# Performance work log

Hardware: AMD Instinct MI355X
Metric: run time of the kernel (lower is better)

## Reference

```python
import jax, jax.numpy as jnp
import numpy as np

NEG = -1000000000.0
EPS = 1e-05

def setup_inputs() -> dict:
    key = jax.random.key(0)
    k1, k2, k3, k4, k5 = jax.random.split(key, 5)
    B, L, E, Q = 64, 2048, 512, 256
    encoded_vecs = jax.random.normal(k1, (B, L, E), dtype=jnp.float32)
    query = jax.random.normal(k2, (B, Q), dtype=jnp.float32)
    length = jax.random.randint(k3, (B,), 1, L + 1, dtype=jnp.int32)
    # Xavier-normal-ish params
    W1 = jax.random.normal(k4, (E + Q, E), dtype=jnp.float32) * jnp.sqrt(2.0 / (E + Q + E))
    b1 = jnp.zeros((E,), dtype=jnp.float32)
    v = jax.random.normal(k5, (E,), dtype=jnp.float32) * jnp.sqrt(2.0 / (E + 1))
    return {"encoded_vecs": encoded_vecs, "query": query, "length": length,
            "W1": W1, "b1": b1, "v": v}

def reference(encoded_vecs, query, length, W1, b1, v):
    B, L, E = encoded_vecs.shape
    # broadcast 2D query over the length dim (repeat in torch code)
    q = jnp.broadcast_to(query[:, None, :], (B, L, query.shape[-1]))
    h = jnp.concatenate([encoded_vecs, q], axis=2)            # [B, L, E+Q]
    u = jnp.tanh(jnp.einsum('blc,ce->ble', h, W1) + b1)       # [B, L, E]
    logits = jnp.einsum('ble,e->bl', u, v)                    # [B, L]
    # masked softmax (faithful to masked_softmax in source)
    mask = (jnp.arange(L)[None, :] < length[:, None])         # [B, L] bool
    masked_logits = jnp.where(mask, logits, NEG)
    max_logits = jnp.max(masked_logits, axis=1, keepdims=True)
    exps = jnp.exp(masked_logits - max_logits) * mask.astype(logits.dtype)
    attention = exps / (jnp.sum(exps, axis=1, keepdims=True) + EPS)  # [B, L]
    context = jnp.einsum('bl,ble->be', attention, encoded_vecs)      # [B, E]
    return (context, attention)
```

## Files before the change

### kernel.cpp

```cpp
#include <hip/hip_runtime.h>

typedef __attribute__((ext_vector_type(4))) float float4v;
typedef __attribute__((ext_vector_type(2))) float float2v;
typedef __attribute__((ext_vector_type(8))) short short8;
typedef __attribute__((ext_vector_type(4))) float f32x4;

#define NEGV (-1000000000.0f)

#define MTOT (64 * 2048)

__device__ __forceinline__ unsigned short f2bf(float f) {
    unsigned int u = __float_as_uint(f);
    u += 0x7fffu + ((u >> 16) & 1u);
    return (unsigned short)(u >> 16);
}

__device__ __forceinline__ void gload_lds16(const void* g, void* l) {
    __builtin_amdgcn_global_load_lds(
        (__attribute__((address_space(1))) unsigned int*)(unsigned long long)(g),
        (__attribute__((address_space(3))) unsigned int*)(unsigned int)(unsigned long long)(l),
        16, 0, 0);
}

__global__ __launch_bounds__(256)
void init_kernel(const float* __restrict__ b1, float* __restrict__ qc,
                 float* __restrict__ ctxraw, float* __restrict__ S) {
    int i = blockIdx.x * 256 + threadIdx.x;
    if (i < 32768) {
        qc[i] = b1[i & 511];
    } else {
        ctxraw[i - 32768] = 0.f;
    }
    if (i < 64) S[i] = 0.f;
}

__global__ __launch_bounds__(256)
void prep_wt_kernel(const float* __restrict__ W1, unsigned short* __restrict__ Wt) {
    __shared__ float t[32][33];
    int bx = blockIdx.x & 15;
    int by = blockIdx.x >> 4;
    int tx = threadIdx.x & 31;
    int ty = threadIdx.x >> 5;
    #pragma unroll
    for (int i = 0; i < 4; ++i)
        t[ty + 8 * i][tx] = W1[(bx * 32 + ty + 8 * i) * 512 + by * 32 + tx];
    __syncthreads();
    #pragma unroll
    for (int i = 0; i < 4; ++i)
        Wt[(by * 32 + ty + 8 * i) * 512 + bx * 32 + tx] = f2bf(t[tx][ty + 8 * i]);
}

__global__ __launch_bounds__(256)
void prep_qc_kernel(const float* __restrict__ query, const float* __restrict__ W1,
                    float* __restrict__ qc) {
    int blk = blockIdx.x;
    int b = blk >> 2;
    int q0 = (blk & 3) * 64;
    int e = threadIdx.x;
    float acc0 = 0.f, acc1 = 0.f;
    const float* w = W1 + (512 + q0) * 512;
    const float* qv = query + b * 256 + q0;
    #pragma unroll 8
    for (int q = 0; q < 64; ++q) {
        float x = qv[q];
        acc0 += x * w[q * 512 + e];
        acc1 += x * w[q * 512 + e + 256];
    }
    atomicAdd(&qc[b * 512 + e], acc0);
    atomicAdd(&qc[b * 512 + e + 256], acc1);
}

__global__ __launch_bounds__(1024)
void gemm_fused_kernel(const float* __restrict__ A,
                       const unsigned short* __restrict__ Wt,
                       const float* __restrict__ qc,
                       const float* __restrict__ v,
                       const int* __restrict__ length,
                       float* __restrict__ att,
                       float* __restrict__ ctxraw,
                       float* __restrict__ S)
{
    int bm = blockIdx.x;
    int b = bm >> 4;
    int len = length[b];
    int l0 = (bm & 15) * 128;
    if (l0 >= len) return;

    __shared__ char smem[139264];
    unsigned short* As = (unsigned short*)smem;
    unsigned short* Bs = (unsigned short*)(smem + 8192);
    float (*lred)[8] = (float(*)[8])(smem + 8192);
    float* wbuf = (float*)(smem + 8192 + 4096);

    int tid = threadIdx.x;
    int lane = tid & 63;
    int w = tid >> 6;
    int wm = w >> 3, wn = w & 7;
    long row0 = (long)bm * 128;

    int ar_r = tid >> 3;
    int ar_e = tid & 7;
    const char* gAr = (const char*)A + (row0 + ar_r) * 2048 + ar_e * 16;
    int awr = ar_r * 64 + ((ar_e * 8) ^ (((ar_r >> 1) & 3) << 4));

    int offw = w * 2048 + lane * 16;
    const char* gB0;
    const char* gB1;
    {
        int o = offw;
        int r = o >> 6;
        gB0 = (const char*)Wt + r * 1024 + ((o & 63) ^ (((r >> 1) & 3) << 4));
        o = offw + 1024;
        r = o >> 6;
        gB1 = (const char*)Wt + r * 1024 + ((o & 63) ^ (((r >> 1) & 3) << 4));
    }

    int aoff[4], boff[4];
    int kb = 16 * (lane >> 4);
    #pragma unroll
    for (int mi = 0; mi < 4; ++mi) {
        int ar = wm * 64 + (lane & 15) + mi * 16;
        aoff[mi] = ar * 64 + (kb ^ (((ar >> 1) & 3) << 4));
    }
    #pragma unroll
    for (int ni = 0; ni < 4; ++ni) {
        int br = wn * 64 + (lane & 15) + ni * 16;
        boff[ni] = br * 64 + (kb ^ (((br >> 1) & 3) << 4));
    }

    f32x4 acc[4][4] = {};
    float4v Pa, Pb;

#define ALOAD(t_, P_) do { P_ = *(const float4v*)(gAr + (t_) * 128); } while (0)

#define BISSUE(t_, sI) do {                                                  \
    char* lb_ = (char*)Bs + (sI) * 32768 + offw;                             \
    gload_lds16(gB0 + (t_) * 64, lb_);                                       \
    gload_lds16(gB1 + (t_) * 64, lb_ + 1024);                                \
} while (0)

#define CVTW(P_) do {                                                        \
    union { unsigned int u[2]; unsigned long long ll; } pk_;                 \
    pk_.u[0] = (unsigned int)f2bf(P_[0]) | ((unsigned int)f2bf(P_[1]) << 16); \
    pk_.u[1] = (unsigned int)f2bf(P_[2]) | ((unsigned int)f2bf(P_[3]) << 16); \
    *(unsigned long long*)((char*)As + awr) = pk_.ll;                        \
} while (0)

#define KCOMP(sC) do {                                                       \
    const char* as_ = (const char*)As;                                       \
    const char* bs_ = (const char*)Bs + (sC) * 32768;                        \
    short8 af_[4];                                                           \
    _Pragma("unroll")                                                        \
    for (int mi = 0; mi < 4; ++mi) af_[mi] = *(const short8*)(as_ + aoff[mi]); \
    _Pragma("unroll")                                                        \
    for (int ni = 0; ni < 4; ++ni) {                                         \
        short8 bf_ = *(const short8*)(bs_ + boff[ni]);                       \
        _Pragma("unroll")                                                    \
        for (int mi = 0; mi < 4; ++mi)                                       \
            acc[mi][ni] = __builtin_amdgcn_mfma_f32_16x16x32_bf16(af_[mi], bf_, acc[mi][ni], 0, 0, 0); \
    }                                                                        \
} while (0)

#define KITER(t, PI, PC, AISS, BISS, VM) do {                                \
    if (AISS) ALOAD((t) + 2, PI);                                            \
    if (BISS) BISSUE((t) + 3, ((t) + 3) & 3);                                \
    KCOMP((t) & 3);                                                          \
    asm volatile("" ::: "memory");                                           \
    __builtin_amdgcn_s_barrier();                                            \
    asm volatile("s_waitcnt vmcnt(" #VM ")" ::: "memory");                   \
    CVTW(PC);                                                                \
    asm volatile("s_waitcnt lgkmcnt(0)" ::: "memory");                       \
    __builtin_amdgcn_s_barrier();                                            \
    asm volatile("" ::: "memory");                                           \
} while (0)

    ALOAD(0, Pa);
    ALOAD(1, Pb);
    BISSUE(0, 0);
    BISSUE(1, 1);
    BISSUE(2, 2);
    asm volatile("s_waitcnt vmcnt(4)" ::: "memory");
    CVTW(Pa);
    asm volatile("s_waitcnt lgkmcnt(0)" ::: "memory");
    __builtin_amdgcn_s_barrier();
    asm volatile("" ::: "memory");

    KITER(0,  Pa, Pb, 1, 1, 5);
    KITER(1,  Pb, Pa, 1, 1, 5);
    KITER(2,  Pa, Pb, 1, 1, 5);
    KITER(3,  Pb, Pa, 1, 1, 5);
    KITER(4,  Pa, Pb, 1, 1, 5);
    KITER(5,  Pb, Pa, 1, 1, 5);
    KITER(6,  Pa, Pb, 1, 1, 5);
    KITER(7,  Pb, Pa, 1, 1, 5);
    KITER(8,  Pa, Pb, 1, 1, 5);
    KITER(9,  Pb, Pa, 1, 1, 5);
    KITER(10, Pa, Pb, 1, 1, 5);
    KITER(11, Pb, Pa, 1, 1, 5);
    KITER(12, Pa, Pb, 1, 1, 5);
    KITER(13, Pb, Pa, 1, 0, 3);
    KITER(14, Pa, Pb, 0, 0, 0);
    KCOMP(3);

    const float* qcb = qc + b * 512;
    float vcol[4], qcol[4];
    #pragma unroll
    for (int ni = 0; ni < 4; ++ni) {
        int c = wn * 64 + ni * 16 + (lane & 15);
        vcol[ni] = v[c];
        qcol[ni] = qcb[c];
    }
    #pragma unroll
    for (int mi = 0; mi < 4; ++mi) {
        #pragma unroll
        for (int j2 = 0; j2 < 4; ++j2) {
            float s = 0.f;
            #pragma unroll
            for (int ni = 0; ni < 4; ++ni) {
                float xx = acc[mi][ni][j2] + qcol[ni];
                float e2 = __expf(2.0f * xx);
                float tt = 1.0f - 2.0f * __builtin_amdgcn_rcpf(e2 + 1.0f);
                s += tt * vcol[ni];
            }
            s += __shfl_xor(s, 1);
            s += __shfl_xor(s, 2);
            s += __shfl_xor(s, 4);
            s += __shfl_xor(s, 8);
            if ((lane & 15) == 0)
                lred[wm * 64 + mi * 16 + 4 * (lane >> 4) + j2][wn] = s;
        }
    }
    __syncthreads();

    if (tid < 128) {
        float lg = 0.f;
        #pragma unroll
        for (int q = 0; q < 8; ++q) lg += lred[tid][q];
        float wf = (l0 + tid < len) ? __expf(lg) : 0.f;
        att[row0 + tid] = wf;
        wbuf[tid] = wf;
        float s = wf;
        #pragma unroll
        for (int m = 32; m; m >>= 1) s += __shfl_xor(s, m);
        if ((tid & 63) == 0) atomicAdd(&S[b], s);
    }
    __syncthreads();

    {
        int e = tid & 511;
        int lh = tid >> 9;
        const float* encb = A + (row0 + lh * 64) * 512 + e;
        const float* wb = &wbuf[lh * 64];
        float c = 0.f;
        #pragma unroll 4
        for (int l = 0; l < 64; ++l)
            c += wb[l] * encb[l * 512];
        atomicAdd(&ctxraw[b * 512 + e], c);
    }
}

__global__ void norm_kernel(const float* __restrict__ S, const int* __restrict__ length,
                            const float* __restrict__ ctxraw,
                            float* __restrict__ att, float* __restrict__ ctx) {
    int b = blockIdx.x;
    int tid = threadIdx.x;
    float inv = 1.0f / S[b];
    ctx[b * 512 + tid] = ctxraw[b * 512 + tid] * inv;
    ctx[b * 512 + 256 + tid] = ctxraw[b * 512 + 256 + tid] * inv;
    int len = length[b];
    float* ab = att + b * 2048;
    #pragma unroll
    for (int i = 0; i < 8; ++i) {
        int l = tid + i * 256;
        float wv = ab[l];
        ab[l] = (l < len) ? wv * inv : 0.f;
    }
}

extern "C" void kernel_launch(void* const* d_in, const int* in_sizes, int n_in,
                              void* d_out, int out_size, void* d_ws, size_t ws_size,
                              hipStream_t stream) {
    const float* enc    = (const float*)d_in[0];
    const float* query  = (const float*)d_in[1];
    const int*   length = (const int*)d_in[2];
    const float* W1     = (const float*)d_in[3];
    const float* b1     = (const float*)d_in[4];
    const float* v      = (const float*)d_in[5];

    float* out = (float*)d_out;
    float* ctx = out;
    float* att = out + 64 * 512;

    char* ws = (char*)d_ws;
    float* qc          = (float*)ws;
    unsigned short* Wt = (unsigned short*)(ws + 64 * 512 * 4);
    float* ctxraw      = (float*)(ws + 64 * 512 * 4 + 512 * 1024);
    float* S           = (float*)(ws + 64 * 512 * 4 + 512 * 1024 + 64 * 512 * 4);

    init_kernel<<<256, 256, 0, stream>>>(b1, qc, ctxraw, S);
    prep_wt_kernel<<<256, 256, 0, stream>>>(W1, Wt);
    prep_qc_kernel<<<256, 256, 0, stream>>>(query, W1, qc);

    gemm_fused_kernel<<<1024, 1024, 0, stream>>>(enc, Wt, qc, v, length, att, ctxraw, S);

    norm_kernel<<<64, 256, 0, stream>>>(S, length, ctxraw, att, ctx);
}
```

Before: 134.8 us.

## Process two K-steps per barrier pair with double-buffered A tile

The GEMM main loop is restructured so that each phase computes two K-steps between one pair of workgroup barriers, rather than one K-step per barrier pair. The A tile in shared memory becomes double-buffered so that two bf16 A slices can be converted and stored per phase. Four A register prefetch buffers are used, and shared memory grows to hold the extra A slice. The aim is to halve the barrier and wait overhead in the 1024-thread workgroup. In exchange, B tiles are now prefetched only one phase ahead instead of three single steps ahead, so more global-load latency may be exposed, and register pressure rises.

Result: faster. 126.0 us (-6.5%).

```diff
diff --git a/kernel.cpp b/kernel.cpp
--- a/kernel.cpp
+++ b/kernel.cpp
@@ -86,11 +86,11 @@
     int l0 = (bm & 15) * 128;
     if (l0 >= len) return;
 
-    __shared__ char smem[139264];
+    __shared__ char smem[147456];
     unsigned short* As = (unsigned short*)smem;
-    unsigned short* Bs = (unsigned short*)(smem + 8192);
-    float (*lred)[8] = (float(*)[8])(smem + 8192);
-    float* wbuf = (float*)(smem + 8192 + 4096);
+    unsigned short* Bs = (unsigned short*)(smem + 16384);
+    float (*lred)[8] = (float(*)[8])(smem + 16384);
+    float* wbuf = (float*)(smem + 16384 + 4096);
 
     int tid = threadIdx.x;
     int lane = tid & 63;
@@ -129,7 +129,7 @@
     }
 
     f32x4 acc[4][4] = {};
-    float4v Pa, Pb;
+    float4v Pa, Pb, Pc, Pd;
 
 #define ALOAD(t_, P_) do { P_ = *(const float4v*)(gAr + (t_) * 128); } while (0)
 
@@ -139,16 +139,16 @@
     gload_lds16(gB1 + (t_) * 64, lb_ + 1024);                                \
 } while (0)
 
-#define CVTW(P_) do {                                                        \
+#define CVTW(P_, sW) do {                                                    \
     union { unsigned int u[2]; unsigned long long ll; } pk_;                 \
     pk_.u[0] = (unsigned int)f2bf(P_[0]) | ((unsigned int)f2bf(P_[1]) << 16); \
     pk_.u[1] = (unsigned int)f2bf(P_[2]) | ((unsigned int)f2bf(P_[3]) << 16); \
-    *(unsigned long long*)((char*)As + awr) = pk_.ll;                        \
+    *(unsigned long long*)((char*)As + (sW) * 8192 + awr) = pk_.ll;          \
 } while (0)
 
-#define KCOMP(sC) do {                                                       \
-    const char* as_ = (const char*)As;                                       \
-    const char* bs_ = (const char*)Bs + (sC) * 32768;                        \
+#define KCOMP(sA, sB) do {                                                   \
+    const char* as_ = (const char*)As + (sA) * 8192;                         \
+    const char* bs_ = (const char*)Bs + (sB) * 32768;                        \
     short8 af_[4];                                                           \
     _Pragma("unroll")                                                        \
     for (int mi = 0; mi < 4; ++mi) af_[mi] = *(const short8*)(as_ + aoff[mi]); \
@@ -161,14 +161,17 @@
     }                                                                        \
 } while (0)
 
-#define KITER(t, PI, PC, AISS, BISS, VM) do {                                \
-    if (AISS) ALOAD((t) + 2, PI);                                            \
-    if (BISS) BISSUE((t) + 3, ((t) + 3) & 3);                                \
-    KCOMP((t) & 3);                                                          \
+#define PHASE(p, PI0, PI1, PC0, PC1, AISS, VM) do {                          \
+    BISSUE(2*(p)+2, (2*(p)+2) & 3);                                          \
+    BISSUE(2*(p)+3, (2*(p)+3) & 3);                                          \
+    if (AISS) { ALOAD(2*(p)+4, PI0); ALOAD(2*(p)+5, PI1); }                  \
+    KCOMP(0, (2*(p)) & 3);                                                   \
+    KCOMP(1, (2*(p)+1) & 3);                                                 \
     asm volatile("" ::: "memory");                                           \
     __builtin_amdgcn_s_barrier();                                            \
     asm volatile("s_waitcnt vmcnt(" #VM ")" ::: "memory");                   \
-    CVTW(PC);                                                                \
+    CVTW(PC0, 0);                                                            \
+    CVTW(PC1, 1);                                                            \
     asm volatile("s_waitcnt lgkmcnt(0)" ::: "memory");                       \
     __builtin_amdgcn_s_barrier();                                            \
     asm volatile("" ::: "memory");                                           \
@@ -178,29 +181,24 @@
     ALOAD(1, Pb);
     BISSUE(0, 0);
     BISSUE(1, 1);
-    BISSUE(2, 2);
-    asm volatile("s_waitcnt vmcnt(4)" ::: "memory");
-    CVTW(Pa);
+    ALOAD(2, Pc);
+    ALOAD(3, Pd);
+    asm volatile("s_waitcnt vmcnt(2)" ::: "memory");
+    CVTW(Pa, 0);
+    CVTW(Pb, 1);
     asm volatile("s_waitcnt lgkmcnt(0)" ::: "memory");
     __builtin_amdgcn_s_barrier();
     asm volatile("" ::: "memory");
 
-    KITER(0,  Pa, Pb, 1, 1, 5);
-    KITER(1,  Pb, Pa, 1, 1, 5);
-    KITER(2,  Pa, Pb, 1, 1, 5);
-    KITER(3,  Pb, Pa, 1, 1, 5);
-    KITER(4,  Pa, Pb, 1, 1, 5);
-    KITER(5,  Pb, Pa, 1, 1, 5);
-    KITER(6,  Pa, Pb, 1, 1, 5);
-    KITER(7,  Pb, Pa, 1, 1, 5);
-    KITER(8,  Pa, Pb, 1, 1, 5);
-    KITER(9,  Pb, Pa, 1, 1, 5);
-    KITER(10, Pa, Pb, 1, 1, 5);
-    KITER(11, Pb, Pa, 1, 1, 5);
-    KITER(12, Pa, Pb, 1, 1, 5);
-    KITER(13, Pb, Pa, 1, 0, 3);
-    KITER(14, Pa, Pb, 0, 0, 0);
-    KCOMP(3);
+    PHASE(0, Pa, Pb, Pc, Pd, 1, 2);
+    PHASE(1, Pc, Pd, Pa, Pb, 1, 2);
+    PHASE(2, Pa, Pb, Pc, Pd, 1, 2);
+    PHASE(3, Pc, Pd, Pa, Pb, 1, 2);
+    PHASE(4, Pa, Pb, Pc, Pd, 1, 2);
+    PHASE(5, Pc, Pd, Pa, Pb, 1, 2);
+    PHASE(6, Pa, Pb, Pc, Pd, 0, 0);
+    KCOMP(0, 2);
+    KCOMP(1, 3);
 
     const float* qcb = qc + b * 512;
     float vcol[4], qcol[4];
```
